# Kernel tuning notes

Hardware: AMD Instinct MI355X
Metric: run time of the kernel (lower is better)

## Reference

```python
import jax, jax.numpy as jnp
import numpy as np

N_NODES = 50000
N_EDGES = 1600000
IN_CH = 256
LAT = 32
HID = 64
OUT_CH = 256
GAT_H = 32  # GAT hidden dims [32, 32], heads=1


def setup_inputs() -> dict:
    key = jax.random.key(0)
    ks = jax.random.split(key, 30)
    nrm = lambda k, shape, s=0.05: jax.random.normal(k, shape, dtype=jnp.float32) * s
    inp = {}
    inp["x"] = jax.random.normal(ks[0], (N_NODES, IN_CH), dtype=jnp.float32)
    inp["edge_index"] = jax.random.randint(ks[1], (2, N_EDGES), 0, N_NODES)
    # GAT layer 1: IN_CH -> 32 (heads=1), layer 2: 32 -> 32, final linear 32 -> LAT
    inp["W_g1"] = nrm(ks[2], (IN_CH, GAT_H)); inp["as_g1"] = nrm(ks[3], (GAT_H,)); inp["ad_g1"] = nrm(ks[4], (GAT_H,)); inp["b_g1"] = jnp.zeros((GAT_H,), jnp.float32)
    inp["W_g2"] = nrm(ks[5], (GAT_H, GAT_H)); inp["as_g2"] = nrm(ks[6], (GAT_H,)); inp["ad_g2"] = nrm(ks[7], (GAT_H,)); inp["b_g2"] = jnp.zeros((GAT_H,), jnp.float32)
    inp["W_gf"] = nrm(ks[8], (GAT_H, LAT)); inp["b_gf"] = jnp.zeros((LAT,), jnp.float32)
    inp["W_m1"] = nrm(ks[9], (IN_CH, HID)); inp["b_m1"] = jnp.zeros((HID,), jnp.float32); inp["g_m1"] = jnp.ones((HID,), jnp.float32); inp["be_m1"] = jnp.zeros((HID,), jnp.float32)
    inp["W_m2"] = nrm(ks[10], (HID, HID)); inp["b_m2"] = jnp.zeros((HID,), jnp.float32); inp["g_m2"] = jnp.ones((HID,), jnp.float32); inp["be_m2"] = jnp.zeros((HID,), jnp.float32)
    inp["W_m3"] = nrm(ks[11], (HID, LAT)); inp["b_m3"] = jnp.zeros((LAT,), jnp.float32); inp["g_m3"] = jnp.ones((LAT,), jnp.float32); inp["be_m3"] = jnp.zeros((LAT,), jnp.float32)
    # final linear LAT -> OUT_CH + ReLU
    inp["W_f"] = nrm(ks[12], (LAT, OUT_CH)); inp["b_f"] = jnp.zeros((OUT_CH,), jnp.float32)
    return inp


def _bn_relu(h, g, b):
    # BatchNorm1d in training mode: batch stats, biased variance, eps=1e-5
    m = jnp.mean(h, axis=0)
    v = jnp.var(h, axis=0)
    return jax.nn.relu((h - m) * jax.lax.rsqrt(v + 1e-5) * g + b)


def _gat(h_in, src, dst, W, a_s, a_d, b):
    # PyG GATConv (heads=1): edge (src j -> dst i), e = LeakyReLU(a_src.Wx_j + a_dst.Wx_i)
    N = h_in.shape[0]
    h = h_in @ W                                   # [N, F]
    e = jax.nn.leaky_relu((h @ a_s)[src] + (h @ a_d)[dst], 0.2)  # [E]
    m = jax.ops.segment_max(e, dst, num_segments=N)              # scatter-softmax over incoming edges
    ex = jnp.exp(e - m[dst])
    den = jax.ops.segment_sum(ex, dst, num_segments=N)
    alpha = ex / den[dst]
    out = jax.ops.segment_sum(alpha[:, None] * h[src], dst, num_segments=N)
    return out + b


def reference(x, edge_index, W_g1, as_g1, ad_g1, b_g1, W_g2, as_g2, ad_g2, b_g2, W_gf, b_gf, W_m1, b_m1, g_m1, be_m1, W_m2, b_m2, g_m2, be_m2, W_m3, b_m3, g_m3, be_m3, W_f, b_f):
    N = x.shape[0]
    loops = jnp.arange(N)
    src = jnp.concatenate([edge_index[0], loops])  # PyG add_self_loops=True
    dst = jnp.concatenate([edge_index[1], loops])
    r = _bn_relu(x @ W_m1 + b_m1, g_m1, be_m1)
    r = _bn_relu(r @ W_m2 + b_m2, g_m2, be_m2)
    r = _bn_relu(r @ W_m3 + b_m3, g_m3, be_m3)
    # GAT interpolation branch (dropout inactive in eval)
    h = jax.nn.relu(_gat(x, src, dst, W_g1, as_g1, ad_g1, b_g1))
    h = jax.nn.relu(_gat(h, src, dst, W_g2, as_g2, ad_g2, b_g2))
    h = h @ W_gf + b_gf
    # blend with alphas = 0.5 constant vector
    out = 0.5 * r + 0.5 * h
    return jax.nn.relu(out @ W_f + b_f)
```

## Files before the change

kernel.cpp:

```cpp
#include <hip/hip_runtime.h>

#define NNODES 50000
#define NEDGES 1600000
#define NBUCK 196
#define BIN_CH 4096
#define CNT_CH 4096

typedef __attribute__((ext_vector_type(4))) float f32x4;
typedef __attribute__((ext_vector_type(8))) short short8;

__device__ __forceinline__ float leaky02(float x) { return x > 0.f ? x : 0.2f * x; }

__device__ __forceinline__ int block_incl_scan(int v, int* sh) {
  int t = threadIdx.x;
  sh[t] = v;
  __syncthreads();
  for (int d = 1; d < 256; d <<= 1) {
    int u = (t >= d) ? sh[t - d] : 0;
    __syncthreads();
    sh[t] += u;
    __syncthreads();
  }
  return sh[t];
}

__global__ __launch_bounds__(256) void k_b0(const int* __restrict__ dst,
                                            int* __restrict__ gcnt, int E) {
  __shared__ int hist[256];
  int t = threadIdx.x;
  hist[t] = 0;
  __syncthreads();
  int base0 = blockIdx.x * CNT_CH;
#pragma unroll
  for (int r = 0; r < CNT_CH / 256; ++r) {
    int idx = base0 + r * 256 + t;
    if (idx < E) atomicAdd(&hist[dst[idx] >> 8], 1);
  }
  __syncthreads();
  if (t < NBUCK && hist[t]) atomicAdd(&gcnt[t], hist[t]);
}

__global__ __launch_bounds__(256) void k_b1(const int* __restrict__ gcnt,
                                            int* __restrict__ base,
                                            int* __restrict__ cursor) {
  __shared__ int sh[256];
  int t = threadIdx.x;
  int v = (t < NBUCK) ? gcnt[t] : 0;
  int incl = block_incl_scan(v, sh);
  if (t < NBUCK) {
    base[t] = incl - v;
    cursor[t] = incl - v;
  }
  if (t == 255) base[NBUCK] = NEDGES;
}

__global__ __launch_bounds__(256) void k_bin(const int* __restrict__ src,
                                             const int* __restrict__ dst,
                                             int* __restrict__ cursor,
                                             unsigned* __restrict__ binned, int E) {
  __shared__ int hist[256];
  __shared__ int cur[256];
  int t = threadIdx.x;
  int base0 = blockIdx.x * BIN_CH;
  unsigned pk[BIN_CH / 256];
  hist[t] = 0;
  __syncthreads();
#pragma unroll
  for (int r = 0; r < BIN_CH / 256; ++r) {
    int idx = base0 + r * 256 + t;
    if (idx < E) {
      unsigned p = ((unsigned)dst[idx] << 16) | (unsigned)src[idx];
      pk[r] = p;
      atomicAdd(&hist[p >> 24], 1);
    }
  }
  __syncthreads();
  if (t < NBUCK && hist[t]) cur[t] = atomicAdd(&cursor[t], hist[t]);
  __syncthreads();
#pragma unroll
  for (int r = 0; r < BIN_CH / 256; ++r) {
    int idx = base0 + r * 256 + t;
    if (idx < E) {
      unsigned p = pk[r];
      int pos = atomicAdd(&cur[p >> 24], 1);
      binned[pos] = p;
    }
  }
}

__global__ __launch_bounds__(256) void k_sort(const unsigned* __restrict__ binned,
                                              const int* __restrict__ base,
                                              int* __restrict__ deg,
                                              int* __restrict__ offs,
                                              int* __restrict__ csr) {
  __shared__ int hist[256];
  __shared__ int scanbuf[256];
  __shared__ int cur[256];
  int t = threadIdx.x;
  int b = blockIdx.x;
  int lo = base[b], hi = base[b + 1];
  int node0 = b << 8;
  hist[t] = 0;
  __syncthreads();
  for (int i = lo + t; i < hi; i += 256)
    atomicAdd(&hist[(binned[i] >> 16) & 255], 1);
  __syncthreads();
  int h = hist[t];
  int incl = block_incl_scan(h, scanbuf);
  int excl = incl - h;
  int node = node0 + t;
  if (node < NNODES) {
    deg[node] = h;
    offs[node] = lo + excl;
  }
  cur[t] = lo + excl;
  __syncthreads();
  for (int i = lo + t; i < hi; i += 256) {
    unsigned p = binned[i];
    int pos = atomicAdd(&cur[(p >> 16) & 255], 1);
    csr[pos] = (int)(p & 0xFFFFu);
  }
}

template <int K, int NC, int TN, int SPLIT, bool BN, bool STATS, int ROWS>
__global__ __launch_bounds__(256) void k_gemm(
    const float* __restrict__ A, const float* __restrict__ bn_sum,
    const float* __restrict__ bn_sq, const float* __restrict__ bn_gamma,
    const float* __restrict__ bn_beta, float invM,
    const float* __restrict__ B0, const float* __restrict__ B1,
    const float* __restrict__ bias0,
    float* __restrict__ out0, float* __restrict__ out1,
    float* __restrict__ gsum, float* __restrict__ gsq, int M) {
  constexpr int KC = 64;
  constexpr int RPT = ROWS / 16;
  __shared__ float As[ROWS * KC];
  __shared__ float Bs[KC * NC];
  __shared__ float scS[BN ? K : 4];
  __shared__ float shS[BN ? K : 4];
  const int tid = threadIdx.x;
  const int row0 = blockIdx.x * ROWS;
  const int cg = tid & 15;
  const int rowg = (tid >> 4) & 15;
  const int swz = (rowg & 3) << 2;

  if constexpr (BN) {
    if (tid < K) {
      float mean = bn_sum[tid] * invM;
      float var = bn_sq[tid] * invM - mean * mean;
      float rs = rsqrtf(var + 1e-5f);
      float sc = rs * bn_gamma[tid];
      scS[tid] = sc;
      shS[tid] = bn_beta[tid] - mean * sc;
    }
    __syncthreads();
  }

  float acc[RPT][TN];
#pragma unroll
  for (int r = 0; r < RPT; ++r)
#pragma unroll
    for (int j = 0; j < TN; ++j) acc[r][j] = 0.f;

  constexpr int KB = KC / 4;
  for (int k0 = 0; k0 < K; k0 += KC) {
#pragma unroll
    for (int it = 0; it < (ROWS * KB) / 256; ++it) {
      int idx = tid + it * 256;
      int row = idx / KB;
      int kb = idx % KB;
      float4 v = make_float4(0.f, 0.f, 0.f, 0.f);
      int grow = row0 + row;
      if (grow < M) {
        v = *reinterpret_cast<const float4*>(&A[(size_t)grow * K + k0 + kb * 4]);
        if constexpr (BN) {
          int kb4 = k0 + kb * 4;
          float4 sc = *reinterpret_cast<const float4*>(&scS[kb4]);
          float4 sf = *reinterpret_cast<const float4*>(&shS[kb4]);
          v.x = fmaxf(v.x * sc.x + sf.x, 0.f);
          v.y = fmaxf(v.y * sc.y + sf.y, 0.f);
          v.z = fmaxf(v.z * sc.z + sf.z, 0.f);
          v.w = fmaxf(v.w * sc.w + sf.w, 0.f);
        }
      }
      *reinterpret_cast<float4*>(&As[row * KC + ((kb ^ (row & 3)) * 4)]) = v;
    }
    {
      constexpr int KB0 = SPLIT / 4;
#pragma unroll
      for (int it = 0; it < (KC * KB0) / 256; ++it) {
        int idx = tid + it * 256;
        int kk = idx / KB0;
        int cb = idx % KB0;
        float4 v = *reinterpret_cast<const float4*>(&B0[(size_t)(k0 + kk) * SPLIT + cb * 4]);
        *reinterpret_cast<float4*>(&Bs[kk * NC + cb * 4]) = v;
      }
    }
    if constexpr (NC > SPLIT) {
      constexpr int W1 = NC - SPLIT;
      constexpr int KB1 = W1 / 4;
#pragma unroll
      for (int it = 0; it < (KC * KB1) / 256; ++it) {
        int idx = tid + it * 256;
        int kk = idx / KB1;
        int cb = idx % KB1;
        float4 v = *reinterpret_cast<const float4*>(&B1[(size_t)(k0 + kk) * W1 + cb * 4]);
        *reinterpret_cast<float4*>(&Bs[kk * NC + SPLIT + cb * 4]) = v;
      }
    }
    __syncthreads();
    for (int kk = 0; kk < KC; kk += 4) {
      float4 a[RPT];
#pragma unroll
      for (int r = 0; r < RPT; ++r)
        a[r] = *reinterpret_cast<const float4*>(&As[(rowg + 16 * r) * KC + (kk ^ swz)]);
      float b[4][TN];
#pragma unroll
      for (int i = 0; i < 4; ++i)
#pragma unroll
        for (int j = 0; j < TN; ++j) b[i][j] = Bs[(kk + i) * NC + cg * TN + j];
#pragma unroll
      for (int r = 0; r < RPT; ++r)
#pragma unroll
        for (int j = 0; j < TN; ++j) {
          acc[r][j] += a[r].x * b[0][j];
          acc[r][j] += a[r].y * b[1][j];
          acc[r][j] += a[r].z * b[2][j];
          acc[r][j] += a[r].w * b[3][j];
        }
    }
    __syncthreads();
  }
  float bias_r[TN];
#pragma unroll
  for (int j = 0; j < TN; ++j) {
    int c = cg * TN + j;
    bias_r[j] = (c < SPLIT) ? bias0[c] : 0.f;
  }
  float cs[TN], cq[TN];
#pragma unroll
  for (int j = 0; j < TN; ++j) { cs[j] = 0.f; cq[j] = 0.f; }
#pragma unroll
  for (int r = 0; r < RPT; ++r) {
    int grow = row0 + rowg + 16 * r;
    if (grow < M) {
#pragma unroll
      for (int j = 0; j < TN; ++j) {
        int c = cg * TN + j;
        if (c < SPLIT) {
          float v = acc[r][j] + bias_r[j];
          out0[(size_t)grow * SPLIT + c] = v;
          if (STATS) { cs[j] += v; cq[j] += v * v; }
        } else {
          out1[(size_t)grow * (NC - SPLIT) + (c - SPLIT)] = acc[r][j];
        }
      }
    }
  }
  if constexpr (STATS) {
#pragma unroll
    for (int j = 0; j < TN; ++j) {
      cs[j] += __shfl_xor(cs[j], 16);
      cs[j] += __shfl_xor(cs[j], 32);
      cq[j] += __shfl_xor(cq[j], 16);
      cq[j] += __shfl_xor(cq[j], 32);
    }
    float* red = Bs;
    int wave = tid >> 6;
    int lane = tid & 63;
    if (lane < 16) {
#pragma unroll
      for (int j = 0; j < TN; ++j) {
        int c = cg * TN + j;
        if (c < SPLIT) {
          red[wave * 2 * SPLIT + c] = cs[j];
          red[wave * 2 * SPLIT + SPLIT + c] = cq[j];
        }
      }
    }
    __syncthreads();
    if (tid < SPLIT) {
      float s = red[tid] + red[2 * SPLIT + tid] + red[4 * SPLIT + tid] + red[6 * SPLIT + tid];
      atomicAdd(&gsum[tid], s);
    } else if (tid < 2 * SPLIT) {
      int c = tid - SPLIT;
      float q = red[SPLIT + c] + red[3 * SPLIT + c] + red[5 * SPLIT + c] + red[7 * SPLIT + c];
      atomicAdd(&gsq[c], q);
    }
  }
}

__global__ __launch_bounds__(512) void k_bsplit(const float* __restrict__ Wm,
                                                const float* __restrict__ Wg,
                                                unsigned short* __restrict__ Bt) {
  int b = blockIdx.x;
  int cc = b / 6, cf = b % 6;
  int t = threadIdx.x;
  int lane = t >> 3, j = t & 7;
  int lg = lane >> 4, lc = lane & 15;
  int k = cc * 32 + lg * 8 + j;
  int col = cf * 16 + lc;
  float v = (col < 64) ? Wm[k * 64 + col] : Wg[k * 32 + (col - 64)];
  unsigned bb = __float_as_uint(v);
  unsigned h = bb & 0xffff0000u;
  float lo = v - __uint_as_float(h);
  Bt[(size_t)(b * 2 + 0) * 512 + t] = (unsigned short)(h >> 16);
  Bt[(size_t)(b * 2 + 1) * 512 + t] = (unsigned short)(__float_as_uint(lo) >> 16);
}

union U16 { uint4 u; short8 s; };
__device__ __forceinline__ short8 as_s8(uint4 u) { U16 t; t.u = u; return t.s; }

__device__ __forceinline__ void split2(float x0, float x1, unsigned& h, unsigned& l) {
  unsigned b0 = __float_as_uint(x0), b1 = __float_as_uint(x1);
  unsigned h0 = b0 & 0xffff0000u, h1 = b1 & 0xffff0000u;
  h = (h0 >> 16) | h1;
  float l0 = x0 - __uint_as_float(h0);
  float l1 = x1 - __uint_as_float(h1);
  l = (__float_as_uint(l0) >> 16) | (__float_as_uint(l1) & 0xffff0000u);
}

__device__ __forceinline__ void split8(const float4& a, const float4& b,
                                       short8& hi, short8& lo) {
  uint4 h, l;
  split2(a.x, a.y, h.x, l.x);
  split2(a.z, a.w, h.y, l.y);
  split2(b.x, b.y, h.z, l.z);
  split2(b.z, b.w, h.w, l.w);
  hi = as_s8(h);
  lo = as_s8(l);
}

__device__ __forceinline__ void gload16(const void* g, void* l) {
  __builtin_amdgcn_global_load_lds(
      (const __attribute__((address_space(1))) void*)g,
      (__attribute__((address_space(3))) void*)l, 16, 0, 0);
}

__global__ __launch_bounds__(512, 2) void k_gemm1_mfma(
    const float* __restrict__ A, const unsigned short* __restrict__ Bt,
    const float* __restrict__ bias0,
    float* __restrict__ out0, float* __restrict__ out1,
    float* __restrict__ gsum, float* __restrict__ gsq, int M) {
  __shared__ unsigned short BsS[49152];
  __shared__ float As[2][128 * 32];
  __shared__ float red[1024];
  const int tid = threadIdx.x;
  const int wv = tid >> 6;
  const int lane = tid & 63;
  const int lg = lane >> 4;
  const int lc = lane & 15;
  const int wr = wv >> 1;
  const int wc = wv & 1;
  const int rowb = blockIdx.x * 128;

  const int srow = lane >> 3;
  const int sfetch = (lane & 7) ^ srow;

  const int rl0 = wr * 32 + lc;
  const int rl1 = rl0 + 16;

  f32x4 acc[2][3];
#pragma unroll
  for (int rf = 0; rf < 2; ++rf)
#pragma unroll
    for (int j = 0; j < 3; ++j) acc[rf][j] = (f32x4){0.f, 0.f, 0.f, 0.f};

  {
    const char* bsrc = (const char*)Bt;
    char* bdst = (char*)BsS;
#pragma unroll
    for (int i = 0; i < 12; ++i) {
      int off = i * 8192 + wv * 1024;
      gload16(bsrc + off + lane * 16, bdst + off);
    }
  }
#pragma unroll
  for (int q = 0; q < 2; ++q) {
    int lrow = wv * 16 + q * 8 + srow;
    int grow = rowb + lrow;
    grow = grow < M ? grow : M - 1;
    gload16(A + (size_t)grow * 256 + sfetch * 4, &As[0][(wv * 16 + q * 8) * 32]);
  }
  __syncthreads();

#pragma unroll
  for (int c = 0; c < 8; ++c) {
    const int buf = c & 1;
    if (c < 7) {
#pragma unroll
      for (int q = 0; q < 2; ++q) {
        int lrow = wv * 16 + q * 8 + srow;
        int grow = rowb + lrow;
        grow = grow < M ? grow : M - 1;
        gload16(A + (size_t)grow * 256 + (c + 1) * 32 + sfetch * 4,
                &As[buf ^ 1][(wv * 16 + q * 8) * 32]);
      }
    }
    uint4 bhr[3], blr[3];
#pragma unroll
    for (int j = 0; j < 3; ++j) {
      const unsigned short* bp = &BsS[((c * 6 + wc * 3 + j) * 2) * 512 + lane * 8];
      bhr[j] = *reinterpret_cast<const uint4*>(bp);
      blr[j] = *reinterpret_cast<const uint4*>(bp + 512);
    }
    float4 a00 = *reinterpret_cast<const float4*>(
        &As[buf][rl0 * 32 + ((2 * lg) ^ (rl0 & 7)) * 4]);
    float4 a01 = *reinterpret_cast<const float4*>(
        &As[buf][rl0 * 32 + ((2 * lg + 1) ^ (rl0 & 7)) * 4]);
    float4 a10 = *reinterpret_cast<const float4*>(
        &As[buf][rl1 * 32 + ((2 * lg) ^ (rl1 & 7)) * 4]);
    float4 a11 = *reinterpret_cast<const float4*>(
        &As[buf][rl1 * 32 + ((2 * lg + 1) ^ (rl1 & 7)) * 4]);
    short8 ah0, al0, ah1, al1;
    split8(a00, a01, ah0, al0);
    split8(a10, a11, ah1, al1);
#pragma unroll
    for (int j = 0; j < 3; ++j) {
      short8 bh = as_s8(bhr[j]), bl = as_s8(blr[j]);
      acc[0][j] = __builtin_amdgcn_mfma_f32_16x16x32_bf16(ah0, bh, acc[0][j], 0, 0, 0);
      acc[0][j] = __builtin_amdgcn_mfma_f32_16x16x32_bf16(al0, bh, acc[0][j], 0, 0, 0);
      acc[0][j] = __builtin_amdgcn_mfma_f32_16x16x32_bf16(ah0, bl, acc[0][j], 0, 0, 0);
      acc[1][j] = __builtin_amdgcn_mfma_f32_16x16x32_bf16(ah1, bh, acc[1][j], 0, 0, 0);
      acc[1][j] = __builtin_amdgcn_mfma_f32_16x16x32_bf16(al1, bh, acc[1][j], 0, 0, 0);
      acc[1][j] = __builtin_amdgcn_mfma_f32_16x16x32_bf16(ah1, bl, acc[1][j], 0, 0, 0);
    }
    __syncthreads();
  }

  red[tid] = 0.f;
  red[tid + 512] = 0.f;
  __syncthreads();

  float bias_r[3];
#pragma unroll
  for (int j = 0; j < 3; ++j) {
    int gcf = wc * 3 + j;
    bias_r[j] = (gcf < 4) ? bias0[gcf * 16 + lc] : 0.f;
  }
  float cs[3] = {0.f, 0.f, 0.f}, cq[3] = {0.f, 0.f, 0.f};
#pragma unroll
  for (int rf = 0; rf < 2; ++rf) {
    int rbase = rowb + wr * 32 + rf * 16 + lg * 4;
#pragma unroll
    for (int i = 0; i < 4; ++i) {
      int row = rbase + i;
      if (row < M) {
#pragma unroll
        for (int j = 0; j < 3; ++j) {
          int gcf = wc * 3 + j;
          if (gcf < 4) {
            float v = acc[rf][j][i] + bias_r[j];
            out0[(size_t)row * 64 + gcf * 16 + lc] = v;
            cs[j] += v;
            cq[j] += v * v;
          } else {
            out1[(size_t)row * 32 + (gcf - 4) * 16 + lc] = acc[rf][j][i];
          }
        }
      }
    }
  }
#pragma unroll
  for (int j = 0; j < 3; ++j) {
    cs[j] += __shfl_xor(cs[j], 16);
    cs[j] += __shfl_xor(cs[j], 32);
    cq[j] += __shfl_xor(cq[j], 16);
    cq[j] += __shfl_xor(cq[j], 32);
  }
  if (lg == 0) {
#pragma unroll
    for (int j = 0; j < 3; ++j) {
      int gcf = wc * 3 + j;
      if (gcf < 4) {
        red[wv * 128 + gcf * 16 + lc] = cs[j];
        red[wv * 128 + 64 + gcf * 16 + lc] = cq[j];
      }
    }
  }
  __syncthreads();
  if (tid < 64) {
    float s = 0.f;
#pragma unroll
    for (int w = 0; w < 8; ++w) s += red[w * 128 + tid];
    atomicAdd(&gsum[tid], s);
  } else if (tid < 128) {
    int cc2 = tid - 64;
    float q = 0.f;
#pragma unroll
    for (int w = 0; w < 8; ++w) q += red[w * 128 + 64 + cc2];
    atomicAdd(&gsq[cc2], q);
  }
}

__global__ __launch_bounds__(256) void k_sdot(const float* __restrict__ g,
                                              const float* __restrict__ as_,
                                              const float* __restrict__ ad_,
                                              float* __restrict__ sv,
                                              float* __restrict__ dv, int N) {
  int lane = threadIdx.x & 31;
  int row = blockIdx.x * 8 + (threadIdx.x >> 5);
  if (row >= N) return;
  float v = g[(size_t)row * 32 + lane];
  float a = v * as_[lane];
  float b = v * ad_[lane];
#pragma unroll
  for (int w = 16; w >= 1; w >>= 1) {
    a += __shfl_xor(a, w);
    b += __shfl_xor(b, w);
  }
  if (lane == 0) {
    sv[row] = a;
    dv[row] = b;
  }
}

__global__ __launch_bounds__(256) void k_gat_agg(
    const float* __restrict__ h, const float* __restrict__ sv,
    const float* __restrict__ dv, const int* __restrict__ offs,
    const int* __restrict__ deg, const int* __restrict__ csr,
    const float* __restrict__ bias, float* __restrict__ out, int N) {
  int lane = threadIdx.x & 31;
  int node = blockIdx.x * 8 + (threadIdx.x >> 5);
  if (node >= N) return;
  int start = offs[node];
  int cnt = deg[node];
  float di = dv[node];
  float ex0 = __expf(leaky02(sv[node] + di));
  float den = ex0;
  float acc = ex0 * h[(size_t)node * 32 + lane];
  int k = 0;
  for (; k + 8 <= cnt; k += 8) {
    int j0 = csr[start + k + 0], j1 = csr[start + k + 1];
    int j2 = csr[start + k + 2], j3 = csr[start + k + 3];
    int j4 = csr[start + k + 4], j5 = csr[start + k + 5];
    int j6 = csr[start + k + 6], j7 = csr[start + k + 7];
    float s0 = sv[j0], s1 = sv[j1], s2 = sv[j2], s3 = sv[j3];
    float s4 = sv[j4], s5 = sv[j5], s6 = sv[j6], s7 = sv[j7];
    float h0 = h[(size_t)j0 * 32 + lane], h1 = h[(size_t)j1 * 32 + lane];
    float h2 = h[(size_t)j2 * 32 + lane], h3 = h[(size_t)j3 * 32 + lane];
    float h4 = h[(size_t)j4 * 32 + lane], h5 = h[(size_t)j5 * 32 + lane];
    float h6 = h[(size_t)j6 * 32 + lane], h7 = h[(size_t)j7 * 32 + lane];
    float e0 = __expf(leaky02(s0 + di)), e1 = __expf(leaky02(s1 + di));
    float e2 = __expf(leaky02(s2 + di)), e3 = __expf(leaky02(s3 + di));
    float e4 = __expf(leaky02(s4 + di)), e5 = __expf(leaky02(s5 + di));
    float e6 = __expf(leaky02(s6 + di)), e7 = __expf(leaky02(s7 + di));
    den += ((e0 + e1) + (e2 + e3)) + ((e4 + e5) + (e6 + e7));
    acc += e0 * h0 + e1 * h1 + e2 * h2 + e3 * h3;
    acc += e4 * h4 + e5 * h5 + e6 * h6 + e7 * h7;
  }
  for (; k < cnt; ++k) {
    int j = csr[start + k];
    float ex = __expf(leaky02(sv[j] + di));
    den += ex;
    acc += ex * h[(size_t)j * 32 + lane];
  }
  out[(size_t)node * 32 + lane] = fmaxf(acc / den + bias[lane], 0.f);
}

__global__ __launch_bounds__(256) void k_small_gemm_sd(
    const float* __restrict__ hin, const float* __restrict__ W,
    const float* __restrict__ as_, const float* __restrict__ ad_,
    float* __restrict__ gout, float* __restrict__ sv, float* __restrict__ dv,
    int N) {
  __shared__ float Ws[32][32];
  {
    int t = threadIdx.x;
#pragma unroll
    for (int r = 0; r < 4; ++r) {
      int idx = t + r * 256;
      Ws[idx >> 5][idx & 31] = W[idx];
    }
  }
  __syncthreads();
  int lane = threadIdx.x & 31;
  int row = blockIdx.x * 8 + (threadIdx.x >> 5);
  if (row >= N) return;
  float hv = hin[(size_t)row * 32 + lane];
  float acc = 0.f;
#pragma unroll
  for (int k = 0; k < 32; ++k) acc += __shfl(hv, k, 32) * Ws[k][lane];
  gout[(size_t)row * 32 + lane] = acc;
  float a = acc * as_[lane];
  float b = acc * ad_[lane];
#pragma unroll
  for (int w = 16; w >= 1; w >>= 1) {
    a += __shfl_xor(a, w);
    b += __shfl_xor(b, w);
  }
  if (lane == 0) {
    sv[row] = a;
    dv[row] = b;
  }
}

__global__ __launch_bounds__(256) void k_final2(
    const float* __restrict__ mlp3, const float* __restrict__ sum3,
    const float* __restrict__ sq3, const float* __restrict__ g3,
    const float* __restrict__ be3, float invM, const float* __restrict__ h2,
    const float* __restrict__ Wgf, const float* __restrict__ bgf,
    const float* __restrict__ Wf, const float* __restrict__ bf,
    float* __restrict__ out, int N) {
  __shared__ float WfS[32 * 256];
  __shared__ float Bl[64][36];
  __shared__ float WgfS[32][33];
  __shared__ float colS[3][32];
  const int t = threadIdx.x;
  const int row0 = blockIdx.x * 64;

  {
    const float4* src = reinterpret_cast<const float4*>(Wf);
    float4* dst = reinterpret_cast<float4*>(WfS);
#pragma unroll
    for (int r = 0; r < 8; ++r) dst[t + r * 256] = src[t + r * 256];
  }
#pragma unroll
  for (int r = 0; r < 4; ++r) {
    int idx = t + r * 256;
    WgfS[idx >> 5][idx & 31] = Wgf[idx];
  }
  if (t < 32) {
    float mean = sum3[t] * invM;
    float var = sq3[t] * invM - mean * mean;
    float rs = rsqrtf(var + 1e-5f);
    float sc = rs * g3[t];
    colS[0][t] = sc;
    colS[1][t] = be3[t] - mean * sc;
    colS[2][t] = bgf[t];
  }
#pragma unroll
  for (int r = 0; r < 2; ++r) {
    int idx = t + r * 256;
    int row = idx >> 3;
    int k4 = idx & 7;
    int grow = row0 + row;
    float4 v = make_float4(0.f, 0.f, 0.f, 0.f);
    if (grow < N) v = *reinterpret_cast<const float4*>(&h2[(size_t)grow * 32 + k4 * 4]);
    *reinterpret_cast<float4*>(&Bl[row][k4 * 4]) = v;
  }
  __syncthreads();

  const int col = t & 31;
  const int rb = t >> 5;
  float w[32];
#pragma unroll
  for (int k = 0; k < 32; ++k) w[k] = WgfS[k][col];
  float bl[8];
#pragma unroll
  for (int r = 0; r < 8; ++r) {
    int row = rb + 8 * r;
    float a = colS[2][col];
#pragma unroll
    for (int k4 = 0; k4 < 8; ++k4) {
      float4 hv = *reinterpret_cast<const float4*>(&Bl[row][k4 * 4]);
      a += hv.x * w[k4 * 4 + 0] + hv.y * w[k4 * 4 + 1] +
           hv.z * w[k4 * 4 + 2] + hv.w * w[k4 * 4 + 3];
    }
    int grow = row0 + row;
    float pre = (grow < N) ? mlp3[(size_t)grow * 32 + col] : 0.f;
    float rv = fmaxf(pre * colS[0][col] + colS[1][col], 0.f);
    bl[r] = 0.5f * rv + 0.5f * a;
  }
  __syncthreads();
#pragma unroll
  for (int r = 0; r < 8; ++r) Bl[rb + 8 * r][col] = bl[r];
  __syncthreads();

  const int cg = t & 31;
  const int rowg = t >> 5;
  const float4* Wf4 = reinterpret_cast<const float4*>(WfS);
  float4 acc0[8], acc1[8];
#pragma unroll
  for (int r = 0; r < 8; ++r) {
    acc0[r] = make_float4(0.f, 0.f, 0.f, 0.f);
    acc1[r] = make_float4(0.f, 0.f, 0.f, 0.f);
  }
  for (int k = 0; k < 32; k += 4) {
    float4 a[8];
#pragma unroll
    for (int r = 0; r < 8; ++r)
      a[r] = *reinterpret_cast<const float4*>(&Bl[rowg + 8 * r][k]);
    float4 b0[4], b1[4];
#pragma unroll
    for (int i = 0; i < 4; ++i) {
      b0[i] = Wf4[(k + i) * 64 + cg];
      b1[i] = Wf4[(k + i) * 64 + cg + 32];
    }
#pragma unroll
    for (int r = 0; r < 8; ++r) {
      float av[4] = {a[r].x, a[r].y, a[r].z, a[r].w};
#pragma unroll
      for (int i = 0; i < 4; ++i) {
        acc0[r].x += av[i] * b0[i].x;
        acc0[r].y += av[i] * b0[i].y;
        acc0[r].z += av[i] * b0[i].z;
        acc0[r].w += av[i] * b0[i].w;
        acc1[r].x += av[i] * b1[i].x;
        acc1[r].y += av[i] * b1[i].y;
        acc1[r].z += av[i] * b1[i].z;
        acc1[r].w += av[i] * b1[i].w;
      }
    }
  }
  float4 bfA = reinterpret_cast<const float4*>(bf)[cg];
  float4 bfB = reinterpret_cast<const float4*>(bf)[cg + 32];
  float4* out4 = reinterpret_cast<float4*>(out);
#pragma unroll
  for (int r = 0; r < 8; ++r) {
    int grow = row0 + rowg + 8 * r;
    if (grow < N) {
      float4 o0 = acc0[r], o1 = acc1[r];
      o0.x = fmaxf(o0.x + bfA.x, 0.f); o0.y = fmaxf(o0.y + bfA.y, 0.f);
      o0.z = fmaxf(o0.z + bfA.z, 0.f); o0.w = fmaxf(o0.w + bfA.w, 0.f);
      o1.x = fmaxf(o1.x + bfB.x, 0.f); o1.y = fmaxf(o1.y + bfB.y, 0.f);
      o1.z = fmaxf(o1.z + bfB.z, 0.f); o1.w = fmaxf(o1.w + bfB.w, 0.f);
      out4[(size_t)grow * 64 + cg] = o0;
      out4[(size_t)grow * 64 + cg + 32] = o1;
    }
  }
}

extern "C" void kernel_launch(void* const* d_in, const int* in_sizes, int n_in,
                              void* d_out, int out_size, void* d_ws, size_t ws_size,
                              hipStream_t stream) {
  const float* x = (const float*)d_in[0];
  const int* edge = (const int*)d_in[1];
  const float* W_g1 = (const float*)d_in[2];
  const float* as_g1 = (const float*)d_in[3];
  const float* ad_g1 = (const float*)d_in[4];
  const float* b_g1 = (const float*)d_in[5];
  const float* W_g2 = (const float*)d_in[6];
  const float* as_g2 = (const float*)d_in[7];
  const float* ad_g2 = (const float*)d_in[8];
  const float* b_g2 = (const float*)d_in[9];
  const float* W_gf = (const float*)d_in[10];
  const float* b_gf = (const float*)d_in[11];
  const float* W_m1 = (const float*)d_in[12];
  const float* b_m1 = (const float*)d_in[13];
  const float* g_m1 = (const float*)d_in[14];
  const float* be_m1 = (const float*)d_in[15];
  const float* W_m2 = (const float*)d_in[16];
  const float* b_m2 = (const float*)d_in[17];
  const float* g_m2 = (const float*)d_in[18];
  const float* be_m2 = (const float*)d_in[19];
  const float* W_m3 = (const float*)d_in[20];
  const float* b_m3 = (const float*)d_in[21];
  const float* g_m3 = (const float*)d_in[22];
  const float* be_m3 = (const float*)d_in[23];
  const float* W_f = (const float*)d_in[24];
  const float* b_f = (const float*)d_in[25];
  float* out = (float*)d_out;

  const int N = NNODES, E = NEDGES;
  const float invM = 1.f / N;
  const int* esrc = edge;
  const int* edst = edge + E;

  float* ws = (float*)d_ws;
  float* g1 = ws;
  float* mlp1 = g1 + (size_t)N * 32;
  float* mlp2 = mlp1 + (size_t)N * 64;
  float* mlp3 = mlp2 + (size_t)N * 64;
  float* h1 = mlp3 + (size_t)N * 32;
  float* g2 = h1 + (size_t)N * 32;
  float* h2 = g2 + (size_t)N * 32;
  float* s1 = h2 + (size_t)N * 32;
  float* d1 = s1 + N;
  float* s2 = d1 + N;
  float* d2 = s2 + N;
  float* stats = d2 + N;
  float* sum1 = stats, *sq1 = stats + 64;
  float* sum2 = stats + 128, *sq2 = stats + 192;
  float* sum3 = stats + 256, *sq3 = stats + 288;
  int* ip = (int*)(stats + 384);
  int* gcnt = ip;
  int* base = gcnt + 256;
  int* cursor = base + 256;
  int* deg = cursor + 256;
  int* offs = deg + N;
  int* csr = offs + N;
  unsigned* binned = (unsigned*)mlp2;
  unsigned short* Bt = (unsigned short*)((char*)mlp2 + (size_t)E * 4);

  hipMemsetAsync(gcnt, 0, 256 * sizeof(int), stream);
  hipMemsetAsync(stats, 0, 384 * sizeof(float), stream);

  k_bsplit<<<48, 512, 0, stream>>>(W_m1, W_g1, Bt);

  k_b0<<<(E + CNT_CH - 1) / CNT_CH, 256, 0, stream>>>(edst, gcnt, E);
  k_b1<<<1, 256, 0, stream>>>(gcnt, base, cursor);
  k_bin<<<(E + BIN_CH - 1) / BIN_CH, 256, 0, stream>>>(esrc, edst, cursor, binned, E);
  k_sort<<<NBUCK, 256, 0, stream>>>(binned, base, deg, offs, csr);

  const int GB64 = (N + 63) / 64;
  const int GB128 = (N + 127) / 128;

  k_gemm1_mfma<<<GB128, 512, 0, stream>>>(x, Bt, b_m1, mlp1, g1, sum1, sq1, N);
  k_sdot<<<(N + 7) / 8, 256, 0, stream>>>(g1, as_g1, ad_g1, s1, d1, N);
  k_gat_agg<<<(N + 7) / 8, 256, 0, stream>>>(g1, s1, d1, offs, deg, csr, b_g1, h1, N);

  k_gemm<64, 64, 4, 64, true, true, 128><<<GB128, 256, 0, stream>>>(
      mlp1, sum1, sq1, g_m1, be_m1, invM, W_m2, nullptr, b_m2,
      mlp2, nullptr, sum2, sq2, N);

  k_small_gemm_sd<<<(N + 7) / 8, 256, 0, stream>>>(h1, W_g2, as_g2, ad_g2, g2, s2, d2, N);
  k_gat_agg<<<(N + 7) / 8, 256, 0, stream>>>(g2, s2, d2, offs, deg, csr, b_g2, h2, N);

  k_gemm<64, 32, 2, 32, true, true, 128><<<GB128, 256, 0, stream>>>(
      mlp2, sum2, sq2, g_m2, be_m2, invM, W_m3, nullptr, b_m3,
      mlp3, nullptr, sum3, sq3, N);

  k_final2<<<(N + 63) / 64, 256, 0, stream>>>(mlp3, sum3, sq3, g_m3, be_m3, invM,
                                              h2, W_gf, b_gf, W_f, b_f, out, N);
}
```

Before: 396.7 us.

## Use split-bf16 MFMA for final GEMM and stream B tiles in gemm1

The final 32->256 projection in k_final2 now uses MFMA bf16 instructions with a hi/lo split (three products per tile) in place of scalar FP32 FMAs, with the W_f weights pre-split by a new small kernel. The first GEMM moves to 64-row blocks of 256 threads and double-buffers per-chunk B tiles instead of loading the whole split weight matrix into LDS. This cuts LDS use so more blocks can be resident. The split-bf16 trick approximates FP32 accuracy, and the output stores become 16-wide strided writes that coalesce less well than the old float4 stores.

```diff
diff --git a/kernel.cpp b/kernel.cpp
--- a/kernel.cpp
+++ b/kernel.cpp
@@ -307,6 +307,22 @@
   Bt[(size_t)(b * 2 + 1) * 512 + t] = (unsigned short)(__float_as_uint(lo) >> 16);
 }
 
+__global__ __launch_bounds__(512) void k_bsplit2(const float* __restrict__ Wf,
+                                                 unsigned short* __restrict__ WfT) {
+  int cf = blockIdx.x;
+  int t = threadIdx.x;
+  int lane = t >> 3, j = t & 7;
+  int lg = lane >> 4, lc = lane & 15;
+  int k = lg * 8 + j;
+  int col = cf * 16 + lc;
+  float v = Wf[k * 256 + col];
+  unsigned bb = __float_as_uint(v);
+  unsigned h = bb & 0xffff0000u;
+  float lo = v - __uint_as_float(h);
+  WfT[(size_t)(cf * 2 + 0) * 512 + t] = (unsigned short)(h >> 16);
+  WfT[(size_t)(cf * 2 + 1) * 512 + t] = (unsigned short)(__float_as_uint(lo) >> 16);
+}
+
 union U16 { uint4 u; short8 s; };
 __device__ __forceinline__ short8 as_s8(uint4 u) { U16 t; t.u = u; return t.s; }
 
@@ -336,14 +352,14 @@
       (__attribute__((address_space(3))) void*)l, 16, 0, 0);
 }
 
-__global__ __launch_bounds__(512, 2) void k_gemm1_mfma(
+__global__ __launch_bounds__(256) void k_gemm1_mfma(
     const float* __restrict__ A, const unsigned short* __restrict__ Bt,
     const float* __restrict__ bias0,
     float* __restrict__ out0, float* __restrict__ out1,
     float* __restrict__ gsum, float* __restrict__ gsq, int M) {
-  __shared__ unsigned short BsS[49152];
-  __shared__ float As[2][128 * 32];
-  __shared__ float red[1024];
+  __shared__ float As[2][64 * 32];
+  __shared__ __align__(16) unsigned short Bs[2][6144];
+  __shared__ float red[512];
   const int tid = threadIdx.x;
   const int wv = tid >> 6;
   const int lane = tid & 63;
@@ -351,7 +367,7 @@
   const int lc = lane & 15;
   const int wr = wv >> 1;
   const int wc = wv & 1;
-  const int rowb = blockIdx.x * 128;
+  const int rowb = blockIdx.x * 64;
 
   const int srow = lane >> 3;
   const int sfetch = (lane & 7) ^ srow;
@@ -365,21 +381,17 @@
 #pragma unroll
     for (int j = 0; j < 3; ++j) acc[rf][j] = (f32x4){0.f, 0.f, 0.f, 0.f};
 
-  {
-    const char* bsrc = (const char*)Bt;
-    char* bdst = (char*)BsS;
-#pragma unroll
-    for (int i = 0; i < 12; ++i) {
-      int off = i * 8192 + wv * 1024;
-      gload16(bsrc + off + lane * 16, bdst + off);
-    }
-  }
 #pragma unroll
   for (int q = 0; q < 2; ++q) {
     int lrow = wv * 16 + q * 8 + srow;
     int grow = rowb + lrow;
     grow = grow < M ? grow : M - 1;
     gload16(A + (size_t)grow * 256 + sfetch * 4, &As[0][(wv * 16 + q * 8) * 32]);
+  }
+#pragma unroll
+  for (int i = 0; i < 3; ++i) {
+    int off = (wv * 3 + i) * 1024;
+    gload16((const char*)Bt + off + lane * 16, (char*)Bs[0] + off);
   }
   __syncthreads();
 
@@ -395,11 +407,17 @@
         gload16(A + (size_t)grow * 256 + (c + 1) * 32 + sfetch * 4,
                 &As[buf ^ 1][(wv * 16 + q * 8) * 32]);
       }
+#pragma unroll
+      for (int i = 0; i < 3; ++i) {
+        int off = (wv * 3 + i) * 1024;
+        gload16((const char*)Bt + (size_t)(c + 1) * 12288 + off + lane * 16,
+                (char*)Bs[buf ^ 1] + off);
+      }
     }
     uint4 bhr[3], blr[3];
 #pragma unroll
     for (int j = 0; j < 3; ++j) {
-      const unsigned short* bp = &BsS[((c * 6 + wc * 3 + j) * 2) * 512 + lane * 8];
+      const unsigned short* bp = &Bs[buf][((wc * 3 + j) * 2) * 512 + lane * 8];
       bhr[j] = *reinterpret_cast<const uint4*>(bp);
       blr[j] = *reinterpret_cast<const uint4*>(bp + 512);
     }
@@ -428,7 +446,7 @@
   }
 
   red[tid] = 0.f;
-  red[tid + 512] = 0.f;
+  red[tid + 256] = 0.f;
   __syncthreads();
 
   float bias_r[3];
@@ -479,16 +497,10 @@
   }
   __syncthreads();
   if (tid < 64) {
-    float s = 0.f;
-#pragma unroll
-    for (int w = 0; w < 8; ++w) s += red[w * 128 + tid];
-    atomicAdd(&gsum[tid], s);
+    atomicAdd(&gsum[tid], red[tid] + red[128 + tid] + red[256 + tid] + red[384 + tid]);
   } else if (tid < 128) {
     int cc2 = tid - 64;
-    float q = 0.f;
-#pragma unroll
-    for (int w = 0; w < 8; ++w) q += red[w * 128 + 64 + cc2];
-    atomicAdd(&gsq[cc2], q);
+    atomicAdd(&gsq[cc2], red[64 + cc2] + red[192 + cc2] + red[320 + cc2] + red[448 + cc2]);
   }
 }
 
@@ -598,26 +610,35 @@
     const float* __restrict__ sq3, const float* __restrict__ g3,
     const float* __restrict__ be3, float invM, const float* __restrict__ h2,
     const float* __restrict__ Wgf, const float* __restrict__ bgf,
-    const float* __restrict__ Wf, const float* __restrict__ bf,
+    const unsigned short* __restrict__ WfT, const float* __restrict__ bf,
     float* __restrict__ out, int N) {
-  __shared__ float WfS[32 * 256];
+  __shared__ __align__(16) unsigned short WfS[16384];
   __shared__ float Bl[64][36];
   __shared__ float WgfS[32][33];
   __shared__ float colS[3][32];
+  __shared__ float bfS[256];
+  __shared__ __align__(16) unsigned short blAh[4][64][8];
+  __shared__ __align__(16) unsigned short blAl[4][64][8];
   const int t = threadIdx.x;
+  const int wv = t >> 6;
+  const int lane = t & 63;
   const int row0 = blockIdx.x * 64;
 
   {
-    const float4* src = reinterpret_cast<const float4*>(Wf);
-    float4* dst = reinterpret_cast<float4*>(WfS);
-#pragma unroll
-    for (int r = 0; r < 8; ++r) dst[t + r * 256] = src[t + r * 256];
+    const char* src = (const char*)WfT;
+    char* dst = (char*)WfS;
+#pragma unroll
+    for (int i = 0; i < 8; ++i) {
+      int off = (i * 4 + wv) * 1024;
+      gload16(src + off + lane * 16, dst + off);
+    }
   }
 #pragma unroll
   for (int r = 0; r < 4; ++r) {
     int idx = t + r * 256;
     WgfS[idx >> 5][idx & 31] = Wgf[idx];
   }
+  bfS[t] = bf[t];
   if (t < 32) {
     float mean = sum3[t] * invM;
     float var = sq3[t] * invM - mean * mean;
@@ -644,7 +665,8 @@
   float w[32];
 #pragma unroll
   for (int k = 0; k < 32; ++k) w[k] = WgfS[k][col];
-  float bl[8];
+  const int lpos = 16 * (col >> 3);
+  const int jj = col & 7;
 #pragma unroll
   for (int r = 0; r < 8; ++r) {
     int row = rb + 8 * r;
@@ -658,63 +680,37 @@
     int grow = row0 + row;
     float pre = (grow < N) ? mlp3[(size_t)grow * 32 + col] : 0.f;
     float rv = fmaxf(pre * colS[0][col] + colS[1][col], 0.f);
-    bl[r] = 0.5f * rv + 0.5f * a;
-  }
-  __syncthreads();
-#pragma unroll
-  for (int r = 0; r < 8; ++r) Bl[rb + 8 * r][col] = bl[r];
-  __syncthreads();
-
-  const int cg = t & 31;
-  const int rowg = t >> 5;
-  const float4* Wf4 = reinterpret_cast<const float4*>(WfS);
-  float4 acc0[8], acc1[8];
-#pragma unroll
-  for (int r = 0; r < 8; ++r) {
-    acc0[r] = make_float4(0.f, 0.f, 0.f, 0.f);
-    acc1[r] = make_float4(0.f, 0.f, 0.f, 0.f);
-  }
-  for (int k = 0; k < 32; k += 4) {
-    float4 a[8];
-#pragma unroll
-    for (int r = 0; r < 8; ++r)
-      a[r] = *reinterpret_cast<const float4*>(&Bl[rowg + 8 * r][k]);
-    float4 b0[4], b1[4];
+    float v = 0.5f * rv + 0.5f * a;
+    int rf = row >> 4;
+    int l = (row & 15) + lpos;
+    unsigned hh = __float_as_uint(v) & 0xffff0000u;
+    blAh[rf][l][jj] = (unsigned short)(hh >> 16);
+    blAl[rf][l][jj] = (unsigned short)(__float_as_uint(v - __uint_as_float(hh)) >> 16);
+  }
+  __syncthreads();
+
+  short8 ah = as_s8(*reinterpret_cast<const uint4*>(&blAh[wv][lane][0]));
+  short8 al = as_s8(*reinterpret_cast<const uint4*>(&blAl[wv][lane][0]));
+  f32x4 acc[16];
+#pragma unroll
+  for (int cf = 0; cf < 16; ++cf) acc[cf] = (f32x4){0.f, 0.f, 0.f, 0.f};
+#pragma unroll
+  for (int cf = 0; cf < 16; ++cf) {
+    short8 bh = as_s8(*reinterpret_cast<const uint4*>(&WfS[(cf * 2) * 512 + lane * 8]));
+    short8 bl_ = as_s8(*reinterpret_cast<const uint4*>(&WfS[(cf * 2 + 1) * 512 + lane * 8]));
+    acc[cf] = __builtin_amdgcn_mfma_f32_16x16x32_bf16(ah, bh, acc[cf], 0, 0, 0);
+    acc[cf] = __builtin_amdgcn_mfma_f32_16x16x32_bf16(al, bh, acc[cf], 0, 0, 0);
+    acc[cf] = __builtin_amdgcn_mfma_f32_16x16x32_bf16(ah, bl_, acc[cf], 0, 0, 0);
+  }
+  const int lg = lane >> 4, lc = lane & 15;
+#pragma unroll
+  for (int cf = 0; cf < 16; ++cf) {
+    float bb = bfS[cf * 16 + lc];
 #pragma unroll
     for (int i = 0; i < 4; ++i) {
-      b0[i] = Wf4[(k + i) * 64 + cg];
-      b1[i] = Wf4[(k + i) * 64 + cg + 32];
-    }
-#pragma unroll
-    for (int r = 0; r < 8; ++r) {
-      float av[4] = {a[r].x, a[r].y, a[r].z, a[r].w};
-#pragma unroll
-      for (int i = 0; i < 4; ++i) {
-        acc0[r].x += av[i] * b0[i].x;
-        acc0[r].y += av[i] * b0[i].y;
-        acc0[r].z += av[i] * b0[i].z;
-        acc0[r].w += av[i] * b0[i].w;
-        acc1[r].x += av[i] * b1[i].x;
-        acc1[r].y += av[i] * b1[i].y;
-        acc1[r].z += av[i] * b1[i].z;
-        acc1[r].w += av[i] * b1[i].w;
-      }
-    }
-  }
-  float4 bfA = reinterpret_cast<const float4*>(bf)[cg];
-  float4 bfB = reinterpret_cast<const float4*>(bf)[cg + 32];
-  float4* out4 = reinterpret_cast<float4*>(out);
-#pragma unroll
-  for (int r = 0; r < 8; ++r) {
-    int grow = row0 + rowg + 8 * r;
-    if (grow < N) {
-      float4 o0 = acc0[r], o1 = acc1[r];
-      o0.x = fmaxf(o0.x + bfA.x, 0.f); o0.y = fmaxf(o0.y + bfA.y, 0.f);
-      o0.z = fmaxf(o0.z + bfA.z, 0.f); o0.w = fmaxf(o0.w + bfA.w, 0.f);
-      o1.x = fmaxf(o1.x + bfB.x, 0.f); o1.y = fmaxf(o1.y + bfB.y, 0.f);
-      o1.z = fmaxf(o1.z + bfB.z, 0.f); o1.w = fmaxf(o1.w + bfB.w, 0.f);
-      out4[(size_t)grow * 64 + cg] = o0;
-      out4[(size_t)grow * 64 + cg + 32] = o1;
+      int row = row0 + wv * 16 + lg * 4 + i;
+      if (row < N)
+        out[(size_t)row * 256 + cf * 16 + lc] = fmaxf(acc[cf][i] + bb, 0.f);
     }
   }
 }
@@ -780,11 +776,13 @@
   int* csr = offs + N;
   unsigned* binned = (unsigned*)mlp2;
   unsigned short* Bt = (unsigned short*)((char*)mlp2 + (size_t)E * 4);
+  unsigned short* WfT = (unsigned short*)(csr + NEDGES);
 
   hipMemsetAsync(gcnt, 0, 256 * sizeof(int), stream);
   hipMemsetAsync(stats, 0, 384 * sizeof(float), stream);
 
   k_bsplit<<<48, 512, 0, stream>>>(W_m1, W_g1, Bt);
+  k_bsplit2<<<16, 512, 0, stream>>>(W_f, WfT);
 
   k_b0<<<(E + CNT_CH - 1) / CNT_CH, 256, 0, stream>>>(edst, gcnt, E);
   k_b1<<<1, 256, 0, stream>>>(gcnt, base, cursor);
@@ -794,7 +792,7 @@
   const int GB64 = (N + 63) / 64;
   const int GB128 = (N + 127) / 128;
 
-  k_gemm1_mfma<<<GB128, 512, 0, stream>>>(x, Bt, b_m1, mlp1, g1, sum1, sq1, N);
+  k_gemm1_mfma<<<GB64, 256, 0, stream>>>(x, Bt, b_m1, mlp1, g1, sum1, sq1, N);
   k_sdot<<<(N + 7) / 8, 256, 0, stream>>>(g1, as_g1, ad_g1, s1, d1, N);
   k_gat_agg<<<(N + 7) / 8, 256, 0, stream>>>(g1, s1, d1, offs, deg, csr, b_g1, h1, N);
 
@@ -809,6 +807,6 @@
       mlp2, sum2, sq2, g_m2, be_m2, invM, W_m3, nullptr, b_m3,
       mlp3, nullptr, sum3, sq3, N);
 
-  k_final2<<<(N + 63) / 64, 256, 0, stream>>>(mlp3, sum3, sq3, g_m3, be_m3, invM,
-                                              h2, W_gf, b_gf, W_f, b_f, out, N);
-}
+  k_final2<<<GB64, 256, 0, stream>>>(mlp3, sum3, sq3, g_m3, be_m3, invM,
+                                     h2, W_gf, b_gf, WfT, b_f, out, N);
+}
```

Result: no change. 394.5 us (-0.5%).
